# Optimization experiments

Hardware: AMD Instinct MI355X
Metric: run time of the kernel (lower is better)

The kernel has to match this reference:

```python
import jax, jax.numpy as jnp
import numpy as np
from jax import lax

KERNEL_SIZE = 3
SMOOTH_NR = 0.0
SMOOTH_DR = 1e-5


def _box_sum(x, k):
    # 3D box-filter sum with zero padding (matches F.conv3d padding=(k-1)//2),
    # x: [B, C, H, W, D]. 'SAME' padding with odd k and stride 1 == symmetric pad (k-1)//2.
    return lax.reduce_window(x, jnp.array(0.0, x.dtype), lax.add,
                             window_dimensions=(1, 1, k, k, k),
                             window_strides=(1, 1, 1, 1, 1),
                             padding='SAME')


def setup_inputs() -> dict:
    key = jax.random.key(0)
    k1, k2 = jax.random.split(key)
    shape = (2, 1, 192, 192, 192)
    pred = jax.random.uniform(k1, shape, dtype=jnp.float32)
    target = jax.random.uniform(k2, shape, dtype=jnp.float32)
    return {"pred": pred, "target": target}


def reference(pred, target):
    k = KERNEL_SIZE
    kvol = float(k ** 3)
    # Local means of I, J, I^2, J^2, I*J (box filter divided by kernel volume,
    # mirroring the torch code's avg_filt grouped conv over the 5C-channel interm).
    mI = _box_sum(pred, k) / kvol
    mJ = _box_sum(target, k) / kvol
    mII = _box_sum(pred * pred, k) / kvol
    mJJ = _box_sum(target * target, k) / kvol
    mIJ = _box_sum(pred * target, k) / kvol
    # Fused NCC reduction (cc3d_fwd_interm_v1): convert means back to
    # windowed sums-based cross/variance terms using kernel_vol.
    cross = kvol * (mIJ - mI * mJ)
    p_var = kvol * (mII - mI * mI)
    t_var = kvol * (mJJ - mJ * mJ)
    ncc = (cross * cross + SMOOTH_NR) / (t_var * p_var + SMOOTH_DR)
    # reduction='mean', loss is negated squared local ZNCC
    return -jnp.mean(ncc)
```

## Files before the change

### kernel.cpp

```cpp
#include <hip/hip_runtime.h>

#define DIMB 2
#define DIMS 192
#define DPT 4
#define TX 16
#define TY 16
#define HCHUNK 6
#define ROWF 72
#define PLANE_F 1296
#define BUF_F 2816
#define NSEG 11

#define GLOAD_LDS16(gp, lp) __builtin_amdgcn_global_load_lds( \
    (const __attribute__((address_space(1))) void*)(gp),      \
    (__attribute__((address_space(3))) void*)(lp), 16, 0, 0)

__device__ __forceinline__ float ncc_row3(const float (&Pm)[5][DPT],
                                          const float (&Pc)[5][DPT],
                                          const float (&Pn)[5][DPT])
{
    const float inv = 1.0f / 27.0f;
    float acc = 0.f;
#pragma unroll
    for (int j = 0; j < DPT; ++j) {
        const float sI  = Pm[0][j] + Pc[0][j] + Pn[0][j];
        const float sJ  = Pm[1][j] + Pc[1][j] + Pn[1][j];
        const float sII = Pm[2][j] + Pc[2][j] + Pn[2][j];
        const float sJJ = Pm[3][j] + Pc[3][j] + Pn[3][j];
        const float sIJ = Pm[4][j] + Pc[4][j] + Pn[4][j];
        const float uI = sI * inv;
        const float uJ = sJ * inv;
        const float cross = sIJ - uI * sJ;
        const float pvar  = sII - uI * sI;
        const float tvar  = sJJ - uJ * sJ;
        acc += (cross * cross) * __builtin_amdgcn_rcpf(tvar * pvar + 1e-5f);
    }
    return acc;
}

__global__ __launch_bounds__(256)
void FusedLocalNormalizedCrossCorrelationLoss_37838661877790_kernel(
    const float* __restrict__ pred, const float* __restrict__ targ,
    double* __restrict__ acc_out)
{
    __shared__ float L[2][BUF_F];

    const int tx = threadIdx.x, ty = threadIdx.y;
    const int tid = ty * TX + tx;
    const int lane = tid & 63, wv = tid >> 6;
    const int d0b = blockIdx.x * (TX * DPT);
    const int w0  = blockIdx.y * TY;
    const int bz  = blockIdx.z;
    const int b   = bz >> 5;
    const int h0  = (bz & 31) * HCHUNK;

    int   sl[3]; int co[3]; const float* ab[3];
#pragma unroll
    for (int i = 0; i < 3; ++i) {
        const int s = wv + 4 * i;
        const int ss = (s < NSEG) ? s : 0;
        const int fi = ss * 256 + lane * 4;
        const int a  = (fi >= PLANE_F) ? 1 : 0;
        int fi2 = fi - a * PLANE_F;
        if (fi2 > PLANE_F - 1) fi2 = PLANE_F - 1;
        const int r = fi2 / ROWF, c = fi2 % ROWF;
        int gd = d0b - 4 + c;
        gd = gd < 0 ? 0 : (gd > DIMS - 4 ? DIMS - 4 : gd);
        int wr = w0 - 1 + r;
        wr = wr < 0 ? 0 : (wr > DIMS - 1 ? DIMS - 1 : wr);
        sl[i] = ss * 256;
        co[i] = wr * DIMS + gd;
        ab[i] = a ? targ : pred;
    }

    auto stage = [&](int buf, int hh) {
        const int hhc = hh < 0 ? 0 : (hh > DIMS - 1 ? DIMS - 1 : hh);
        const size_t po = ((size_t)b * DIMS + hhc) * (DIMS * DIMS);
#pragma unroll
        for (int i = 0; i < 3; ++i) {
            if (wv + 4 * i >= NSEG) break;
            GLOAD_LDS16(ab[i] + po + co[i], &L[buf][sl[i]]);
        }
    };

    const bool lo_mask = (tx == 0)      && (blockIdx.x == 0);
    const bool hi_mask = (tx == TX - 1) && (blockIdx.x == gridDim.x - 1);
    const int rb0 = 4 * tx;

    auto plane = [&](int buf, int hh, float (&P)[5][DPT]) {
#pragma unroll
        for (int c5 = 0; c5 < 5; ++c5)
#pragma unroll
            for (int j = 0; j < DPT; ++j) P[c5][j] = 0.f;
        if (hh < 0 || hh >= DIMS) return;
        const float* Lp = &L[buf][0];
        const float* Lt = &L[buf][PLANE_F];
#pragma unroll
        for (int dw = 0; dw < 3; ++dw) {
            const int wr = w0 + ty + dw - 1;
            if (wr < 0 || wr >= DIMS) continue;
            const int rb = (ty + dw) * ROWF + rb0;
            float p0 = Lp[rb + 3];
            const float4 pm = *reinterpret_cast<const float4*>(Lp + rb + 4);
            float p5 = Lp[rb + 8];
            float t0 = Lt[rb + 3];
            const float4 tm = *reinterpret_cast<const float4*>(Lt + rb + 4);
            float t5 = Lt[rb + 8];
            if (lo_mask) { p0 = 0.f; t0 = 0.f; }
            if (hi_mask) { p5 = 0.f; t5 = 0.f; }
            const float pv[6] = {p0, pm.x, pm.y, pm.z, pm.w, p5};
            const float tv[6] = {t0, tm.x, tm.y, tm.z, tm.w, t5};
            float pp[6], tt[6], pt[6];
#pragma unroll
            for (int k = 0; k < 6; ++k) {
                pp[k] = pv[k] * pv[k];
                tt[k] = tv[k] * tv[k];
                pt[k] = pv[k] * tv[k];
            }
#pragma unroll
            for (int j = 0; j < DPT; ++j) {
                P[0][j] += pv[j] + pv[j+1] + pv[j+2];
                P[1][j] += tv[j] + tv[j+1] + tv[j+2];
                P[2][j] += pp[j] + pp[j+1] + pp[j+2];
                P[3][j] += tt[j] + tt[j+1] + tt[j+2];
                P[4][j] += pt[j] + pt[j+1] + pt[j+2];
            }
        }
    };

    float PA[5][DPT], PB[5][DPT], PC[5][DPT];
    float acc = 0.f;

    stage(0, h0 - 1);
    stage(1, h0);
    __syncthreads();
    plane(0, h0 - 1, PA);
    __syncthreads();
    stage(0, h0 + 1);
    plane(1, h0, PB);
    __syncthreads();
    stage(1, h0 + 2);
    plane(0, h0 + 1, PC);  acc += ncc_row3(PA, PB, PC);
    __syncthreads();
    stage(0, h0 + 3);
    plane(1, h0 + 2, PA);  acc += ncc_row3(PB, PC, PA);
    __syncthreads();
    stage(1, h0 + 4);
    plane(0, h0 + 3, PB);  acc += ncc_row3(PC, PA, PB);
    __syncthreads();
    stage(0, h0 + 5);
    plane(1, h0 + 4, PC);  acc += ncc_row3(PA, PB, PC);
    __syncthreads();
    stage(1, h0 + 6);
    plane(0, h0 + 5, PA);  acc += ncc_row3(PB, PC, PA);
    __syncthreads();
    plane(1, h0 + 6, PB);  acc += ncc_row3(PC, PA, PB);

#pragma unroll
    for (int off = 32; off > 0; off >>= 1)
        acc += __shfl_down(acc, off, 64);
    __shared__ float wacc[4];
    if ((tid & 63) == 0) wacc[tid >> 6] = acc;
    __syncthreads();
    if (tid == 0) {
        const double s = (double)wacc[0] + (double)wacc[1]
                       + (double)wacc[2] + (double)wacc[3];
        atomicAdd(acc_out, s);
    }
}

__global__ void ncc_finalize(const double* __restrict__ acc,
                             float* __restrict__ out)
{
    const double n = (double)((size_t)DIMB * DIMS * DIMS * DIMS);
    out[0] = (float)(-acc[0] / n);
}

extern "C" void kernel_launch(void* const* d_in, const int* in_sizes, int n_in,
                              void* d_out, int out_size, void* d_ws, size_t ws_size,
                              hipStream_t stream) {
    const float* pred = (const float*)d_in[0];
    const float* targ = (const float*)d_in[1];
    double* acc = (double*)d_ws;

    hipMemsetAsync(d_ws, 0, sizeof(double), stream);

    dim3 block(TX, TY, 1);
    dim3 grid(DIMS / (TX * DPT), DIMS / TY, DIMB * (DIMS / HCHUNK));
    FusedLocalNormalizedCrossCorrelationLoss_37838661877790_kernel
        <<<grid, block, 0, stream>>>(pred, targ, acc);
    ncc_finalize<<<1, 1, 0, stream>>>(acc, (float*)d_out);
}
```

Baseline: 178.3 us.

## Double H chunk per block, use lane permutes for halo, share window partial sums

Each block now processes 12 H planes instead of 6, which cuts the redundant halo-plane loads and box sums per output from 8/6 to 14/12. Fewer blocks are launched as a result. The left and right D-neighbour values now come from ds_bpermute across lanes, and only the edge threads read them from LDS. The 3-wide window sums reuse shared pairwise partials. The trade-off is half as many blocks, which lowers parallelism, plus a longer serial chain of synchronised steps per block.

```diff
diff --git a/kernel.cpp b/kernel.cpp
--- a/kernel.cpp
+++ b/kernel.cpp
@@ -5,7 +5,8 @@
 #define DPT 4
 #define TX 16
 #define TY 16
-#define HCHUNK 6
+#define HCHUNK 12
+#define NP (HCHUNK + 2)
 #define ROWF 72
 #define PLANE_F 1296
 #define BUF_F 2816
@@ -51,8 +52,11 @@
     const int d0b = blockIdx.x * (TX * DPT);
     const int w0  = blockIdx.y * TY;
     const int bz  = blockIdx.z;
-    const int b   = bz >> 5;
-    const int h0  = (bz & 31) * HCHUNK;
+    const int b   = bz >> 4;
+    const int h0  = (bz & 15) * HCHUNK;
+
+    const int bpL = ((tx == 0)      ? lane : lane - 1) << 2;
+    const int bpR = ((tx == TX - 1) ? lane : lane + 1) << 2;
 
     int   sl[3]; int co[3]; const float* ab[3];
 #pragma unroll
@@ -100,12 +104,14 @@
             const int wr = w0 + ty + dw - 1;
             if (wr < 0 || wr >= DIMS) continue;
             const int rb = (ty + dw) * ROWF + rb0;
-            float p0 = Lp[rb + 3];
             const float4 pm = *reinterpret_cast<const float4*>(Lp + rb + 4);
-            float p5 = Lp[rb + 8];
-            float t0 = Lt[rb + 3];
             const float4 tm = *reinterpret_cast<const float4*>(Lt + rb + 4);
-            float t5 = Lt[rb + 8];
+            float p0 = __int_as_float(__builtin_amdgcn_ds_bpermute(bpL, __float_as_int(pm.w)));
+            float p5 = __int_as_float(__builtin_amdgcn_ds_bpermute(bpR, __float_as_int(pm.x)));
+            float t0 = __int_as_float(__builtin_amdgcn_ds_bpermute(bpL, __float_as_int(tm.w)));
+            float t5 = __int_as_float(__builtin_amdgcn_ds_bpermute(bpR, __float_as_int(tm.x)));
+            if (tx == 0)      { p0 = Lp[rb + 3]; t0 = Lt[rb + 3]; }
+            if (tx == TX - 1) { p5 = Lp[rb + 8]; t5 = Lt[rb + 8]; }
             if (lo_mask) { p0 = 0.f; t0 = 0.f; }
             if (hi_mask) { p5 = 0.f; t5 = 0.f; }
             const float pv[6] = {p0, pm.x, pm.y, pm.z, pm.w, p5};
@@ -117,44 +123,37 @@
                 tt[k] = tv[k] * tv[k];
                 pt[k] = pv[k] * tv[k];
             }
-#pragma unroll
-            for (int j = 0; j < DPT; ++j) {
-                P[0][j] += pv[j] + pv[j+1] + pv[j+2];
-                P[1][j] += tv[j] + tv[j+1] + tv[j+2];
-                P[2][j] += pp[j] + pp[j+1] + pp[j+2];
-                P[3][j] += tt[j] + tt[j+1] + tt[j+2];
-                P[4][j] += pt[j] + pt[j+1] + pt[j+2];
-            }
+#define WSUM(dst, a)                                          \
+            { const float c12 = a[1] + a[2], c34 = a[3] + a[4]; \
+              dst[0] += a[0] + c12; dst[1] += c12 + a[3];       \
+              dst[2] += a[2] + c34; dst[3] += c34 + a[5]; }
+            WSUM(P[0], pv)
+            WSUM(P[1], tv)
+            WSUM(P[2], pp)
+            WSUM(P[3], tt)
+            WSUM(P[4], pt)
+#undef WSUM
         }
     };
 
-    float PA[5][DPT], PB[5][DPT], PC[5][DPT];
+    float P[3][5][DPT];
     float acc = 0.f;
 
     stage(0, h0 - 1);
     stage(1, h0);
     __syncthreads();
-    plane(0, h0 - 1, PA);
-    __syncthreads();
-    stage(0, h0 + 1);
-    plane(1, h0, PB);
-    __syncthreads();
-    stage(1, h0 + 2);
-    plane(0, h0 + 1, PC);  acc += ncc_row3(PA, PB, PC);
-    __syncthreads();
-    stage(0, h0 + 3);
-    plane(1, h0 + 2, PA);  acc += ncc_row3(PB, PC, PA);
-    __syncthreads();
-    stage(1, h0 + 4);
-    plane(0, h0 + 3, PB);  acc += ncc_row3(PC, PA, PB);
-    __syncthreads();
-    stage(0, h0 + 5);
-    plane(1, h0 + 4, PC);  acc += ncc_row3(PA, PB, PC);
-    __syncthreads();
-    stage(1, h0 + 6);
-    plane(0, h0 + 5, PA);  acc += ncc_row3(PB, PC, PA);
-    __syncthreads();
-    plane(1, h0 + 6, PB);  acc += ncc_row3(PC, PA, PB);
+
+#define STEP(q)                                                              \
+    {                                                                        \
+        if ((q) >= 1 && (q) + 1 < NP) stage(((q) + 1) & 1, h0 + (q));        \
+        plane((q) & 1, h0 - 1 + (q), P[(q) % 3]);                            \
+        if ((q) >= 2)                                                        \
+            acc += ncc_row3(P[((q) - 2) % 3], P[((q) - 1) % 3], P[(q) % 3]); \
+        if ((q) + 1 < NP) __syncthreads();                                   \
+    }
+    STEP(0)  STEP(1)  STEP(2)  STEP(3)  STEP(4)  STEP(5)  STEP(6)
+    STEP(7)  STEP(8)  STEP(9)  STEP(10) STEP(11) STEP(12) STEP(13)
+#undef STEP
 
 #pragma unroll
     for (int off = 32; off > 0; off >>= 1)
```

Result: slower. 210.9 us (+18.3%).
